# Kernel tuning notes

Hardware: AMD Instinct MI355X
Metric: run time of the kernel (lower is better)

## Reference

```python
import jax, jax.numpy as jnp
import numpy as np

B, T, IN, H, L = 512, 75, 96, 1024, 3
HARDTANH_LIMIT = 1.0


def setup_inputs() -> dict:
    key = jax.random.key(0)
    ks = jax.random.split(key, 32)
    inp = {
        'inputs': jax.random.normal(ks[0], (B, T, IN), jnp.float32),
        'hiddens': jax.random.normal(ks[1], (L, B, H), jnp.float32),
        'cells': jax.random.normal(ks[2], (L, B, H), jnp.float32),
    }
    s = 1.0 / np.sqrt(H)
    kidx = 3
    for i in range(L):
        in_dim = IN if i == 0 else H
        inp[f'Wih{i}'] = jax.random.uniform(ks[kidx], (4 * H, in_dim), jnp.float32, -s, s); kidx += 1
        inp[f'Whh{i}'] = jax.random.uniform(ks[kidx], (4 * H, H), jnp.float32, -s, s); kidx += 1
        inp[f'bih{i}'] = jax.random.uniform(ks[kidx], (4 * H,), jnp.float32, -s, s); kidx += 1
        inp[f'bhh{i}'] = jax.random.uniform(ks[kidx], (4 * H,), jnp.float32, -s, s); kidx += 1
    inp['fc_w'] = jax.random.uniform(ks[kidx], (IN, H), jnp.float32, -s, s); kidx += 1
    inp['fc_b'] = jax.random.uniform(ks[kidx], (IN,), jnp.float32, -s, s)
    return inp


def _lstm_cell(x, h, c, Wih, Whh, bih, bhh):
    # PyTorch LSTMCell gate order: i, f, g, o
    gates = x @ Wih.T + bih + h @ Whh.T + bhh  # [B, 4H]
    i, f, g, o = jnp.split(gates, 4, axis=-1)
    c_new = jax.nn.sigmoid(f) * c + jax.nn.sigmoid(i) * jnp.tanh(g)
    h_new = jax.nn.sigmoid(o) * jnp.tanh(c_new)
    return h_new, c_new


def reference(inputs, hiddens, cells,
              Wih0, Whh0, bih0, bhh0,
              Wih1, Whh1, bih1, bhh1,
              Wih2, Whh2, bih2, bhh2,
              fc_w, fc_b):
    params = [(Wih0, Whh0, bih0, bhh0),
              (Wih1, Whh1, bih1, bhh1),
              (Wih2, Whh2, bih2, bhh2)]
    # dropout p=0.0 -> identity
    out0 = inputs[..., 0, :]  # [B, IN]

    def step(carry, _):
        hs, cs, out = carry
        x = jax.lax.stop_gradient(out)  # .detach() in the original
        new_h, new_c = [], []
        for i, (Wih, Whh, bih, bhh) in enumerate(params):
            xi = x if i == 0 else new_h[i - 1]
            h, c = _lstm_cell(xi, hs[i], cs[i], Wih, Whh, bih, bhh)
            new_h.append(h)
            new_c.append(c)
        out = new_h[-1] @ fc_w.T + fc_b
        out = jnp.clip(out, -HARDTANH_LIMIT, HARDTANH_LIMIT)  # Hardtanh
        return (jnp.stack(new_h), jnp.stack(new_c), out), out

    (_, _, _), outs = jax.lax.scan(step, (hiddens, cells, out0), None, length=inputs.shape[-2])
    return jnp.swapaxes(outs, 0, 1)  # [B, T, IN]
```

## Files before the change

kernel.cpp:

```cpp
#include <hip/hip_runtime.h>
#include <cstdint>
#include <cstddef>


typedef unsigned short u16;
typedef float v4f __attribute__((ext_vector_type(4)));
typedef short v8s __attribute__((ext_vector_type(8)));
typedef u16   v8u16 __attribute__((ext_vector_type(8)));

#define BATCH 512
#define H_DIM 1024
#define GATES 4096
#define T_STEPS 75
#define IN_DIM 96
#define K0P 1152
#define K12 2048

__device__ __forceinline__ float bf2f(u16 u) {
    unsigned int x = ((unsigned int)u) << 16;
    return __builtin_bit_cast(float, x);
}
__device__ __forceinline__ u16 f2bf(float f) {
    unsigned int x = __builtin_bit_cast(unsigned int, f);
    x += 0x7fffu + ((x >> 16) & 1u);
    return (u16)(x >> 16);
}
__device__ __forceinline__ void gload16(const void* g, void* l) {
    __builtin_amdgcn_global_load_lds(
        (const __attribute__((address_space(1))) void*)g,
        (__attribute__((address_space(3))) void*)l, 16, 0, 0);
}

__global__ __launch_bounds__(256, 1) void lstm_layer_k(
    const u16* __restrict__ A, const u16* __restrict__ W, int K, int nsteps,
    const float* __restrict__ bias, float* __restrict__ c,
    u16* __restrict__ h1, int h1s, u16* __restrict__ h2, int h2s)
{
    __shared__ __align__(16) char smem[49152];
    u16* sA = (u16*)smem;
    u16* sB = (u16*)(smem + 16384);

    const int tid  = threadIdx.x;
    const int lane = tid & 63;
    const int wid  = tid >> 6;
    const int wm   = (wid >> 1) * 32;
    const int wn   = (wid & 1) * 64;
    const int l15  = lane & 15;
    const int lq   = lane >> 4;

    const int id    = blockIdx.x;
    const int panel = (id & 7) * 4 + (id >> 6);
    const int mblk  = (id >> 3) & 7;
    const int bm    = mblk * 64;
    const int j0    = panel * 32;

    v4f acc[2][4];
    #pragma unroll
    for (int nf = 0; nf < 4; ++nf) {
        const int ncol = wn + nf * 16 + l15;
        const float bv = bias[(ncol >> 5) * H_DIM + j0 + (ncol & 31)];
        v4f t = {bv, bv, bv, bv};
        acc[0][nf] = t; acc[1][nf] = t;
    }

    const int srow = tid >> 3;
    const int kcs  = ((tid & 7) ^ (srow & 7)) << 3;

    auto stage = [&](int b, int k0) {
        u16* sa = sA + b * 4096;
        u16* sb = sB + b * 8192;
        gload16(A + (size_t)(bm + srow) * K + k0 + kcs,      sa + tid * 8);
        gload16(A + (size_t)(bm + 32 + srow) * K + k0 + kcs, sa + 2048 + tid * 8);
        #pragma unroll
        for (int q = 0; q < 4; ++q)
            gload16(W + (size_t)(q * H_DIM + j0 + srow) * K + k0 + kcs,
                    sb + q * 2048 + tid * 8);
    };

    stage(0, 0);
    #pragma unroll 1
    for (int t = 0; t < nsteps; ++t) {
        const int cur = t & 1;
        if (t + 1 < nsteps) {
            stage(cur ^ 1, (t + 1) * 64);
            asm volatile("s_waitcnt vmcnt(6)" ::: "memory");
        } else {
            asm volatile("s_waitcnt vmcnt(0)" ::: "memory");
        }
        asm volatile("s_barrier" ::: "memory");

        const char* sa = (const char*)(sA + cur * 4096);
        const char* sb = (const char*)(sB + cur * 8192);
        v8s af[2][2], bfr[4][2];
        #pragma unroll
        for (int mf = 0; mf < 2; ++mf)
            #pragma unroll
            for (int ks = 0; ks < 2; ++ks) {
                const int row = wm + mf * 16 + l15;
                const int ch  = ks * 4 + lq;
                af[mf][ks] = *(const v8s*)(sa + row * 128 + (((ch ^ (row & 7))) << 4));
            }
        #pragma unroll
        for (int nf = 0; nf < 4; ++nf)
            #pragma unroll
            for (int ks = 0; ks < 2; ++ks) {
                const int row = wn + nf * 16 + l15;
                const int ch  = ks * 4 + lq;
                bfr[nf][ks] = *(const v8s*)(sb + row * 128 + (((ch ^ (row & 7))) << 4));
            }
        #pragma unroll
        for (int ks = 0; ks < 2; ++ks)
            #pragma unroll
            for (int mf = 0; mf < 2; ++mf)
                #pragma unroll
                for (int nf = 0; nf < 4; ++nf)
                    acc[mf][nf] = __builtin_amdgcn_mfma_f32_16x16x32_bf16(
                        af[mf][ks], bfr[nf][ks], acc[mf][nf], 0, 0, 0);
        asm volatile("s_barrier" ::: "memory");
    }

    float* sG = (float*)smem;
    #pragma unroll
    for (int mf = 0; mf < 2; ++mf)
        #pragma unroll
        for (int nf = 0; nf < 4; ++nf)
            #pragma unroll
            for (int r = 0; r < 4; ++r)
                sG[(wm + mf * 16 + lq * 4 + r) * 132 + wn + nf * 16 + l15] =
                    acc[mf][nf][r];
    __syncthreads();

    const int row = tid >> 2;
    const int jj  = (tid & 3) * 8;
    const int gb  = bm + row;
    const float* sGr = sG + row * 132;
    float* crow = c + (size_t)gb * H_DIM + j0 + jj;
    v4f c0 = *(const v4f*)crow;
    v4f c1 = *(const v4f*)(crow + 4);
    v4f n0, n1;
    v8u16 hv;
    #pragma unroll
    for (int q = 0; q < 8; ++q) {
        const float gi = sGr[      jj + q];
        const float gf = sGr[32  + jj + q];
        const float gg = sGr[64  + jj + q];
        const float go = sGr[96  + jj + q];
        const float cv = (q < 4) ? c0[q] : c1[q - 4];
        const float ii = 1.f / (1.f + __expf(-gi));
        const float ff = 1.f / (1.f + __expf(-gf));
        const float g2 = tanhf(gg);
        const float oo = 1.f / (1.f + __expf(-go));
        const float cq = ff * cv + ii * g2;
        if (q < 4) n0[q] = cq; else n1[q - 4] = cq;
        hv[q] = f2bf(oo * tanhf(cq));
    }
    *(v4f*)crow       = n0;
    *(v4f*)(crow + 4) = n1;
    *(v8u16*)(h1 + (size_t)gb * h1s + j0 + jj) = hv;
    if (h2)
        *(v8u16*)(h2 + (size_t)gb * h2s + j0 + jj) = hv;
}

__global__ __launch_bounds__(128) void fc_k(
    const u16* __restrict__ h2, int h2stride,
    const u16* __restrict__ w, const float* __restrict__ fcb,
    float* __restrict__ out, u16* __restrict__ xdst, int t)
{
    __shared__ float sh[H_DIM];
    const int b = blockIdx.x, tid = threadIdx.x;
    v8u16 hv = *(const v8u16*)(h2 + (size_t)b * h2stride + tid * 8);
    #pragma unroll
    for (int q = 0; q < 8; ++q) sh[tid * 8 + q] = bf2f(hv[q]);
    __syncthreads();
    if (tid < IN_DIM) {
        const u16* wr = w + (size_t)tid * H_DIM;
        float acc = fcb[tid];
        for (int k = 0; k < H_DIM; k += 8) {
            v8u16 wv = *(const v8u16*)(wr + k);
            #pragma unroll
            for (int q = 0; q < 8; ++q) acc += sh[k + q] * bf2f(wv[q]);
        }
        acc = fminf(1.f, fmaxf(-1.f, acc));
        out[(size_t)b * (T_STEPS * IN_DIM) + t * IN_DIM + tid] = acc;
        xdst[(size_t)b * K0P + tid] = f2bf(acc);
    }
}

__global__ __launch_bounds__(256) void convpack_k(
    const float* __restrict__ src, int srcStride,
    u16* __restrict__ dst, int dstStride, int cols8, long total8)
{
    long i = (long)blockIdx.x * 256 + threadIdx.x;
    if (i >= total8) return;
    const int r  = (int)(i / cols8);
    const int cc = (int)(i - (long)r * cols8) * 8;
    const float* s = src + (size_t)r * srcStride + cc;
    v4f a = *(const v4f*)s;
    v4f b = *(const v4f*)(s + 4);
    v8u16 o;
    #pragma unroll
    for (int q = 0; q < 4; ++q) { o[q] = f2bf(a[q]); o[4 + q] = f2bf(b[q]); }
    *(v8u16*)(dst + (size_t)r * dstStride + cc) = o;
}

__global__ __launch_bounds__(256) void zero16_k(
    u16* __restrict__ dst, int dstStride, int cols8, long total8)
{
    long i = (long)blockIdx.x * 256 + threadIdx.x;
    if (i >= total8) return;
    const int r  = (int)(i / cols8);
    const int cc = (int)(i - (long)r * cols8) * 8;
    v8u16 z = {0, 0, 0, 0, 0, 0, 0, 0};
    *(v8u16*)(dst + (size_t)r * dstStride + cc) = z;
}

__global__ __launch_bounds__(256) void add_k(
    const float* __restrict__ a, const float* __restrict__ b,
    float* __restrict__ o, int n)
{
    int i = blockIdx.x * 256 + threadIdx.x;
    if (i < n) o[i] = a[i] + b[i];
}

extern "C" void kernel_launch(void* const* d_in, const int* in_sizes, int n_in,
                              void* d_out, int out_size, void* d_ws, size_t ws_size,
                              hipStream_t stream)
{
    const float* inputs  = (const float*)d_in[0];
    const float* hiddens = (const float*)d_in[1];
    const float* cells   = (const float*)d_in[2];
    const float* Wih[3]  = {(const float*)d_in[3], (const float*)d_in[7],  (const float*)d_in[11]};
    const float* Whh[3]  = {(const float*)d_in[4], (const float*)d_in[8],  (const float*)d_in[12]};
    const float* bih[3]  = {(const float*)d_in[5], (const float*)d_in[9],  (const float*)d_in[13]};
    const float* bhh[3]  = {(const float*)d_in[6], (const float*)d_in[10], (const float*)d_in[14]};
    const float* fc_w    = (const float*)d_in[15];
    const float* fc_b    = (const float*)d_in[16];
    float* out = (float*)d_out;

    char* p = (char*)d_ws;
    auto take = [&](size_t bytes) -> void* {
        void* r = p; p += (bytes + 255) & ~(size_t)255; return r;
    };
    const int Kl[3]  = {K0P, K12, K12};
    const int Kin[3] = {IN_DIM, H_DIM, H_DIM};
    u16* wcat[3];
    for (int l = 0; l < 3; ++l) wcat[l] = (u16*)take((size_t)GATES * Kl[l] * 2);
    u16* Ab[3][2];
    for (int l = 0; l < 3; ++l)
        for (int q = 0; q < 2; ++q) Ab[l][q] = (u16*)take((size_t)BATCH * Kl[l] * 2);
    u16*   fcwb = (u16*)take((size_t)IN_DIM * H_DIM * 2);
    float* bsum = (float*)take((size_t)3 * GATES * 4);
    float* cbuf = (float*)take((size_t)3 * BATCH * H_DIM * 4);
    if ((size_t)(p - (char*)d_ws) > ws_size) return;

    auto pack = [&](const float* s, int ss, u16* d, int ds, int rows, int cols) {
        long t8 = (long)rows * (cols / 8);
        convpack_k<<<(int)((t8 + 255) / 256), 256, 0, stream>>>(s, ss, d, ds, cols / 8, t8);
    };
    auto zero = [&](u16* d, int ds, int rows, int cols) {
        long t8 = (long)rows * (cols / 8);
        zero16_k<<<(int)((t8 + 255) / 256), 256, 0, stream>>>(d, ds, cols / 8, t8);
    };

    for (int l = 0; l < 3; ++l) {
        pack(Wih[l], Kin[l], wcat[l],           Kl[l], GATES, Kin[l]);
        pack(Whh[l], H_DIM,  wcat[l] + Kin[l],  Kl[l], GATES, H_DIM);
    }
    zero(wcat[0] + IN_DIM + H_DIM, K0P, GATES, K0P - IN_DIM - H_DIM);
    pack(fc_w, H_DIM, fcwb, H_DIM, IN_DIM, H_DIM);

    for (int l = 0; l < 3; ++l)
        pack(hiddens + (size_t)l * BATCH * H_DIM, H_DIM,
             Ab[l][0] + Kin[l], Kl[l], BATCH, H_DIM);
    pack(inputs, T_STEPS * IN_DIM, Ab[0][0], K0P, BATCH, IN_DIM);
    zero(Ab[0][0] + IN_DIM + H_DIM, K0P, BATCH, K0P - IN_DIM - H_DIM);
    zero(Ab[0][1] + IN_DIM + H_DIM, K0P, BATCH, K0P - IN_DIM - H_DIM);

    for (int l = 0; l < 3; ++l)
        add_k<<<16, 256, 0, stream>>>(bih[l], bhh[l], bsum + l * GATES, GATES);
    hipMemcpyAsync(cbuf, cells, (size_t)3 * BATCH * H_DIM * 4,
                   hipMemcpyDeviceToDevice, stream);

    for (int t = 0; t < T_STEPS; ++t) {
        const int pr = t & 1, pn = pr ^ 1;
        lstm_layer_k<<<256, 256, 0, stream>>>(
            Ab[0][pr], wcat[0], K0P, K0P / 64, bsum,
            cbuf,
            Ab[0][pn] + IN_DIM, K0P,
            Ab[1][pr], K12);
        lstm_layer_k<<<256, 256, 0, stream>>>(
            Ab[1][pr], wcat[1], K12, K12 / 64, bsum + GATES,
            cbuf + (size_t)BATCH * H_DIM,
            Ab[1][pn] + H_DIM, K12,
            Ab[2][pr], K12);
        lstm_layer_k<<<256, 256, 0, stream>>>(
            Ab[2][pr], wcat[2], K12, K12 / 64, bsum + 2 * GATES,
            cbuf + (size_t)2 * BATCH * H_DIM,
            Ab[2][pn] + H_DIM, K12,
            (u16*)nullptr, 0);
        fc_k<<<BATCH, 128, 0, stream>>>(
            Ab[2][pn] + H_DIM, K12, fcwb, fc_b, out, Ab[0][pn], t);
    }
}
```

Baseline: 4.744 ms.

## Fuse all timesteps into one persistent kernel with software grid barriers

Replaces the 300 per-step kernel launches (three LSTM layers plus FC per timestep) with a single persistent kernel of 256 blocks. Stages are separated by a flag-based grid barrier, and each block keeps its slice of the cell state in registers across all timesteps instead of reading and writing global memory. The aim is to remove launch overhead and the c-state memory traffic. The cost is a barrier that relies on all 256 blocks being co-resident, and spin loops with iteration caps that could break out early and silently give wrong results.

```diff
diff --git a/kernel.cpp b/kernel.cpp
--- a/kernel.cpp
+++ b/kernel.cpp
@@ -15,6 +15,7 @@
 #define IN_DIM 96
 #define K0P 1152
 #define K12 2048
+#define NBLK 256
 
 __device__ __forceinline__ float bf2f(u16 u) {
     unsigned int x = ((unsigned int)u) << 16;
@@ -31,12 +32,52 @@
         (__attribute__((address_space(3))) void*)l, 16, 0, 0);
 }
 
-__global__ __launch_bounds__(256, 1) void lstm_layer_k(
-    const u16* __restrict__ A, const u16* __restrict__ W, int K, int nsteps,
-    const float* __restrict__ bias, float* __restrict__ c,
-    u16* __restrict__ h1, int h1s, u16* __restrict__ h2, int h2s)
-{
-    __shared__ __align__(16) char smem[49152];
+__device__ __forceinline__ void grid_sync(int* flags, int* genp, int id, int g) {
+    __syncthreads();
+    const int tid = threadIdx.x;
+    if (id == 0) {
+        if (tid < 64) {
+            if (tid == 0) {
+                __threadfence();
+                __hip_atomic_store(&flags[0], g, __ATOMIC_RELEASE, __HIP_MEMORY_SCOPE_AGENT);
+            }
+            int spins = 0;
+            for (;;) {
+                int a = __hip_atomic_load(&flags[tid * 4 + 0], __ATOMIC_RELAXED, __HIP_MEMORY_SCOPE_AGENT);
+                int b = __hip_atomic_load(&flags[tid * 4 + 1], __ATOMIC_RELAXED, __HIP_MEMORY_SCOPE_AGENT);
+                int c = __hip_atomic_load(&flags[tid * 4 + 2], __ATOMIC_RELAXED, __HIP_MEMORY_SCOPE_AGENT);
+                int d = __hip_atomic_load(&flags[tid * 4 + 3], __ATOMIC_RELAXED, __HIP_MEMORY_SCOPE_AGENT);
+                bool ok = (a >= g) && (b >= g) && (c >= g) && (d >= g);
+                if (__all(ok)) break;
+                if (++spins > (1 << 16)) break;
+                __builtin_amdgcn_s_sleep(2);
+            }
+            if (tid == 0) {
+                __threadfence();
+                __hip_atomic_store(genp, g, __ATOMIC_RELEASE, __HIP_MEMORY_SCOPE_AGENT);
+            }
+        }
+    } else {
+        if (tid == 0) {
+            __threadfence();
+            __hip_atomic_store(&flags[id], g, __ATOMIC_RELEASE, __HIP_MEMORY_SCOPE_AGENT);
+            int spins = 0;
+            while (__hip_atomic_load(genp, __ATOMIC_RELAXED, __HIP_MEMORY_SCOPE_AGENT) < g) {
+                if (++spins > (1 << 16)) break;
+                __builtin_amdgcn_s_sleep(2);
+            }
+            __threadfence();
+        }
+    }
+    __syncthreads();
+}
+
+__device__ __forceinline__ void gemm_stage(
+    char* smem, const u16* __restrict__ A, const u16* __restrict__ W,
+    int K, int nk, v4f bv, v4f& cA, v4f& cB,
+    u16* __restrict__ h1, int h1s, u16* __restrict__ h2, int h2s,
+    int bm, int j0)
+{
     u16* sA = (u16*)smem;
     u16* sB = (u16*)(smem + 16384);
 
@@ -48,19 +89,11 @@
     const int l15  = lane & 15;
     const int lq   = lane >> 4;
 
-    const int id    = blockIdx.x;
-    const int panel = (id & 7) * 4 + (id >> 6);
-    const int mblk  = (id >> 3) & 7;
-    const int bm    = mblk * 64;
-    const int j0    = panel * 32;
-
     v4f acc[2][4];
     #pragma unroll
     for (int nf = 0; nf < 4; ++nf) {
-        const int ncol = wn + nf * 16 + l15;
-        const float bv = bias[(ncol >> 5) * H_DIM + j0 + (ncol & 31)];
-        v4f t = {bv, bv, bv, bv};
-        acc[0][nf] = t; acc[1][nf] = t;
+        v4f tv = {bv[nf], bv[nf], bv[nf], bv[nf]};
+        acc[0][nf] = tv; acc[1][nf] = tv;
     }
 
     const int srow = tid >> 3;
@@ -79,10 +112,10 @@
 
     stage(0, 0);
     #pragma unroll 1
-    for (int t = 0; t < nsteps; ++t) {
-        const int cur = t & 1;
-        if (t + 1 < nsteps) {
-            stage(cur ^ 1, (t + 1) * 64);
+    for (int tt = 0; tt < nk; ++tt) {
+        const int cur = tt & 1;
+        if (tt + 1 < nk) {
+            stage(cur ^ 1, (tt + 1) * 64);
             asm volatile("s_waitcnt vmcnt(6)" ::: "memory");
         } else {
             asm volatile("s_waitcnt vmcnt(0)" ::: "memory");
@@ -130,13 +163,10 @@
                     acc[mf][nf][r];
     __syncthreads();
 
-    const int row = tid >> 2;
-    const int jj  = (tid & 3) * 8;
-    const int gb  = bm + row;
-    const float* sGr = sG + row * 132;
-    float* crow = c + (size_t)gb * H_DIM + j0 + jj;
-    v4f c0 = *(const v4f*)crow;
-    v4f c1 = *(const v4f*)(crow + 4);
+    const int erow = tid >> 2;
+    const int jj   = (tid & 3) * 8;
+    const int gb   = bm + erow;
+    const float* sGr = sG + erow * 132;
     v4f n0, n1;
     v8u16 hv;
     #pragma unroll
@@ -145,7 +175,7 @@
         const float gf = sGr[32  + jj + q];
         const float gg = sGr[64  + jj + q];
         const float go = sGr[96  + jj + q];
-        const float cv = (q < 4) ? c0[q] : c1[q - 4];
+        const float cv = (q < 4) ? cA[q] : cB[q - 4];
         const float ii = 1.f / (1.f + __expf(-gi));
         const float ff = 1.f / (1.f + __expf(-gf));
         const float g2 = tanhf(gg);
@@ -154,35 +184,105 @@
         if (q < 4) n0[q] = cq; else n1[q - 4] = cq;
         hv[q] = f2bf(oo * tanhf(cq));
     }
-    *(v4f*)crow       = n0;
-    *(v4f*)(crow + 4) = n1;
+    cA = n0; cB = n1;
     *(v8u16*)(h1 + (size_t)gb * h1s + j0 + jj) = hv;
     if (h2)
         *(v8u16*)(h2 + (size_t)gb * h2s + j0 + jj) = hv;
 }
 
-__global__ __launch_bounds__(128) void fc_k(
-    const u16* __restrict__ h2, int h2stride,
+__device__ __forceinline__ void fc_stage(
+    char* smem, const u16* __restrict__ h2, int h2s,
     const u16* __restrict__ w, const float* __restrict__ fcb,
-    float* __restrict__ out, u16* __restrict__ xdst, int t)
-{
-    __shared__ float sh[H_DIM];
-    const int b = blockIdx.x, tid = threadIdx.x;
-    v8u16 hv = *(const v8u16*)(h2 + (size_t)b * h2stride + tid * 8);
-    #pragma unroll
-    for (int q = 0; q < 8; ++q) sh[tid * 8 + q] = bf2f(hv[q]);
+    float* __restrict__ out, u16* __restrict__ xdst, int t, int id)
+{
+    float* sh = (float*)smem;
+    const int tid  = threadIdx.x;
+    const int half = tid >> 7;
+    const int htid = tid & 127;
+    const int b    = id * 2 + half;
+    v8u16 hvv = *(const v8u16*)(h2 + (size_t)b * h2s + htid * 8);
+    #pragma unroll
+    for (int q = 0; q < 8; ++q) sh[half * H_DIM + htid * 8 + q] = bf2f(hvv[q]);
     __syncthreads();
-    if (tid < IN_DIM) {
-        const u16* wr = w + (size_t)tid * H_DIM;
-        float acc = fcb[tid];
+    if (htid < IN_DIM) {
+        const u16* wr = w + (size_t)htid * H_DIM;
+        const float* shr = sh + half * H_DIM;
+        float acc = fcb[htid];
+        #pragma unroll 4
         for (int k = 0; k < H_DIM; k += 8) {
             v8u16 wv = *(const v8u16*)(wr + k);
             #pragma unroll
-            for (int q = 0; q < 8; ++q) acc += sh[k + q] * bf2f(wv[q]);
+            for (int q = 0; q < 8; ++q) acc += shr[k + q] * bf2f(wv[q]);
         }
         acc = fminf(1.f, fmaxf(-1.f, acc));
-        out[(size_t)b * (T_STEPS * IN_DIM) + t * IN_DIM + tid] = acc;
-        xdst[(size_t)b * K0P + tid] = f2bf(acc);
+        out[(size_t)b * (T_STEPS * IN_DIM) + t * IN_DIM + htid] = acc;
+        xdst[(size_t)b * K0P + htid] = f2bf(acc);
+    }
+}
+
+__global__ __launch_bounds__(256, 1) void lstm_all_k(
+    const u16* __restrict__ w0, const u16* __restrict__ w1, const u16* __restrict__ w2,
+    u16* A00, u16* A01, u16* A10, u16* A11, u16* A20, u16* A21,
+    const u16* __restrict__ fcw, const float* __restrict__ bsum,
+    const float* __restrict__ cells, const float* __restrict__ fcb,
+    float* __restrict__ out, int* flags, int* genp)
+{
+    __shared__ __align__(16) char smem[49152];
+
+    const int tid  = threadIdx.x;
+    const int lane = tid & 63;
+    const int wid  = tid >> 6;
+    const int wn   = (wid & 1) * 64;
+    const int l15  = lane & 15;
+
+    const int id    = blockIdx.x;
+    const int panel = (id & 7) * 4 + (id >> 6);
+    const int mblk  = (id >> 3) & 7;
+    const int bm    = mblk * 64;
+    const int j0    = panel * 32;
+
+    v4f bv0, bv1, bv2;
+    #pragma unroll
+    for (int nf = 0; nf < 4; ++nf) {
+        const int ncol = wn + nf * 16 + l15;
+        const int idx  = (ncol >> 5) * H_DIM + j0 + (ncol & 31);
+        bv0[nf] = bsum[idx];
+        bv1[nf] = bsum[GATES + idx];
+        bv2[nf] = bsum[2 * GATES + idx];
+    }
+
+    const int erow = tid >> 2;
+    const int jj   = (tid & 3) * 8;
+    const int gb   = bm + erow;
+    v4f c0a, c0b, c1a, c1b, c2a, c2b;
+    {
+        const float* cr = cells + (size_t)gb * H_DIM + j0 + jj;
+        c0a = *(const v4f*)cr; c0b = *(const v4f*)(cr + 4);
+        cr += (size_t)BATCH * H_DIM;
+        c1a = *(const v4f*)cr; c1b = *(const v4f*)(cr + 4);
+        cr += (size_t)BATCH * H_DIM;
+        c2a = *(const v4f*)cr; c2b = *(const v4f*)(cr + 4);
+    }
+
+    int g = 0;
+    #pragma unroll 1
+    for (int t = 0; t < T_STEPS; ++t) {
+        const int pr = t & 1;
+        u16* A0r = pr ? A01 : A00;  u16* A0w = pr ? A00 : A01;
+        u16* A1r = pr ? A11 : A10;  u16* A1w = pr ? A10 : A11;
+        u16* A2r = pr ? A21 : A20;  u16* A2w = pr ? A20 : A21;
+
+        gemm_stage(smem, A0r, w0, K0P, K0P / 64, bv0, c0a, c0b,
+                   A0w + IN_DIM, K0P, A1r, K12, bm, j0);
+        grid_sync(flags, genp, id, ++g);
+        gemm_stage(smem, A1r, w1, K12, K12 / 64, bv1, c1a, c1b,
+                   A1w + H_DIM, K12, A2r, K12, bm, j0);
+        grid_sync(flags, genp, id, ++g);
+        gemm_stage(smem, A2r, w2, K12, K12 / 64, bv2, c2a, c2b,
+                   A2w + H_DIM, K12, (u16*)nullptr, 0, bm, j0);
+        grid_sync(flags, genp, id, ++g);
+        fc_stage(smem, A2w + H_DIM, K12, fcw, fcb, out, A0w, t, id);
+        grid_sync(flags, genp, id, ++g);
     }
 }
 
@@ -250,7 +350,7 @@
         for (int q = 0; q < 2; ++q) Ab[l][q] = (u16*)take((size_t)BATCH * Kl[l] * 2);
     u16*   fcwb = (u16*)take((size_t)IN_DIM * H_DIM * 2);
     float* bsum = (float*)take((size_t)3 * GATES * 4);
-    float* cbuf = (float*)take((size_t)3 * BATCH * H_DIM * 4);
+    int*   bar  = (int*)take(4096);
     if ((size_t)(p - (char*)d_ws) > ws_size) return;
 
     auto pack = [&](const float* s, int ss, u16* d, int ds, int rows, int cols) {
@@ -278,27 +378,11 @@
 
     for (int l = 0; l < 3; ++l)
         add_k<<<16, 256, 0, stream>>>(bih[l], bhh[l], bsum + l * GATES, GATES);
-    hipMemcpyAsync(cbuf, cells, (size_t)3 * BATCH * H_DIM * 4,
-                   hipMemcpyDeviceToDevice, stream);
-
-    for (int t = 0; t < T_STEPS; ++t) {
-        const int pr = t & 1, pn = pr ^ 1;
-        lstm_layer_k<<<256, 256, 0, stream>>>(
-            Ab[0][pr], wcat[0], K0P, K0P / 64, bsum,
-            cbuf,
-            Ab[0][pn] + IN_DIM, K0P,
-            Ab[1][pr], K12);
-        lstm_layer_k<<<256, 256, 0, stream>>>(
-            Ab[1][pr], wcat[1], K12, K12 / 64, bsum + GATES,
-            cbuf + (size_t)BATCH * H_DIM,
-            Ab[1][pn] + H_DIM, K12,
-            Ab[2][pr], K12);
-        lstm_layer_k<<<256, 256, 0, stream>>>(
-            Ab[2][pr], wcat[2], K12, K12 / 64, bsum + 2 * GATES,
-            cbuf + (size_t)2 * BATCH * H_DIM,
-            Ab[2][pn] + H_DIM, K12,
-            (u16*)nullptr, 0);
-        fc_k<<<BATCH, 128, 0, stream>>>(
-            Ab[2][pn] + H_DIM, K12, fcwb, fc_b, out, Ab[0][pn], t);
-    }
-}
+    hipMemsetAsync(bar, 0, 4096, stream);
+
+    lstm_all_k<<<NBLK, 256, 0, stream>>>(
+        wcat[0], wcat[1], wcat[2],
+        Ab[0][0], Ab[0][1], Ab[1][0], Ab[1][1], Ab[2][0], Ab[2][1],
+        fcwb, bsum, cells, fc_b, out,
+        bar, bar + 320);
+}
```

Result: slower. 8.276 ms (+74.4%).
